# Optimization experiments

Measured on AMD Instinct MI355X. Metric: run time of the kernel, lower is better.

The kernel has to match this reference:

```python
import jax, jax.numpy as jnp
import numpy as np

NUM_EMBEDDINGS = 8192
EMBEDDING_DIM = 512
BATCH = 16384
COMMITMENT_COST = 0.25
EMBEDDING_SCALE = 0.1


def setup_inputs() -> dict:
    key = jax.random.key(0)
    k1, k2 = jax.random.split(key)
    x = jax.random.randint(k1, (BATCH,), 0, NUM_EMBEDDINGS, dtype=jnp.int64 if jax.config.jax_enable_x64 else jnp.int32)
    # codebook initialized uniform(-scale, scale) like the torch module
    W = jax.random.uniform(k2, (NUM_EMBEDDINGS, EMBEDDING_DIM), dtype=jnp.float32,
                           minval=-EMBEDDING_SCALE, maxval=EMBEDDING_SCALE)
    return {"x": x, "W": W}


def reference(x, W):
    # x: (B,) int indices into codebook; W: (K, D) codebook
    x_emb = W[x]                                           # (B, D) gather
    # squared euclidean distances via ||a||^2 + ||b||^2 - 2 a.b  -> (B, K)
    distances = ((x_emb ** 2).sum(axis=1, keepdims=True)
                 + (W ** 2).sum(axis=1)
                 - 2.0 * jnp.einsum('bd,kd->bk', x_emb, W))
    assignments = jnp.argmin(distances, axis=1)            # (B,)
    quantized = W[assignments]                             # (B, D)
    diff = quantized - x_emb                               # (B, D)
    loss = (diff ** 2).sum(axis=1).mean()
    loss = loss + COMMITMENT_COST * (W ** 2).sum()
    return (loss, quantized, diff)
```

## Files before the change

### kernel.cpp

```cpp
#include <hip/hip_runtime.h>

#define NUM_EMB    8192
#define EMB_DIM    512
#define BATCH_N    16384
#define BD         (BATCH_N * EMB_DIM)
#define TOTAL_OUT  (2 * BD + 1)
#define NCHUNK     (TOTAL_OUT / 4)
#define QCHUNK_END (BD / 4)
#define NBLOCKS    2048
#define NTHREADS   256
#define NTOTAL     (NBLOCKS * NTHREADS)

__device__ float g_partial[NBLOCKS];

__global__ __launch_bounds__(NTHREADS) void vq_sum(const float* __restrict__ W) {
    int tid = blockIdx.x * NTHREADS + threadIdx.x;
    const float4* W4 = (const float4*)W;
    float4 a = W4[tid];
    float4 b = W4[tid + NTOTAL];
    float s = a.x*a.x + a.y*a.y + a.z*a.z + a.w*a.w
            + b.x*b.x + b.y*b.y + b.z*b.z + b.w*b.w;
#pragma unroll
    for (int off = 32; off > 0; off >>= 1) s += __shfl_down(s, off, 64);
    __shared__ float ls[NTHREADS / 64];
    if ((threadIdx.x & 63) == 0) ls[threadIdx.x >> 6] = s;
    __syncthreads();
    if (threadIdx.x == 0) g_partial[blockIdx.x] = ls[0] + ls[1] + ls[2] + ls[3];
}

__global__ __launch_bounds__(NTHREADS) void vq_write(const int* __restrict__ x,
        const float* __restrict__ W, float* __restrict__ out) {
    const int tid  = blockIdx.x * NTHREADS + threadIdx.x;
    const int lane = threadIdx.x & 63;
    const int wave = (tid >> 6);
    float4* out4 = (float4*)out;

    const int b0 = 2 * wave;
    const int b1 = 2 * wave + 1;

    int k0 = x[b0];
    int k1 = x[b1];
    int kp = (b0 > 0) ? x[b0 - 1] : 0;

#pragma unroll
    for (int k = 0; k < 4; ++k) {
        int c = QCHUNK_END + 1 + tid + k * NTOTAL;
        if (c < NCHUNK) out4[c] = make_float4(0.f, 0.f, 0.f, 0.f);
    }
    if (blockIdx.x == 1 && threadIdx.x == 0) {
        out[TOTAL_OUT - 1] = 0.0f;
        float w = W[x[BATCH_N - 1] * EMB_DIM + 511];
        out4[QCHUNK_END] = make_float4(w, 0.f, 0.f, 0.f);
    }

    const float4* R0 = (const float4*)(W + k0 * EMB_DIM);
    const float4* R1 = (const float4*)(W + k1 * EMB_DIM);
    float4 a0 = R0[2 * lane], a1 = R0[2 * lane + 1];
    float4 c0 = R1[2 * lane], c1 = R1[2 * lane + 1];
    float p0 = W[kp * EMB_DIM + 511];
    float p1 = W[k0 * EMB_DIM + 511];

    {
        float pw = __shfl_up(a1.w, 1, 64);
        float first = (lane == 0) ? p0 : pw;
        int cb = 128 * b0;
        if (b0 != 0 || lane != 0)
            out4[cb + 2 * lane]     = make_float4(first, a0.x, a0.y, a0.z);
        out4[cb + 2 * lane + 1]     = make_float4(a0.w,  a1.x, a1.y, a1.z);
    }
    {
        float pw = __shfl_up(c1.w, 1, 64);
        float first = (lane == 0) ? p1 : pw;
        int cb = 128 * b1;
        out4[cb + 2 * lane]         = make_float4(first, c0.x, c0.y, c0.z);
        out4[cb + 2 * lane + 1]     = make_float4(c0.w,  c1.x, c1.y, c1.z);
    }

    if (blockIdx.x == 0) {
        __shared__ float red[NTHREADS];
        float s = 0.0f;
        for (int i = threadIdx.x; i < NBLOCKS; i += NTHREADS) s += g_partial[i];
        red[threadIdx.x] = s;
        __syncthreads();
        for (int st = NTHREADS / 2; st > 0; st >>= 1) {
            if (threadIdx.x < st) red[threadIdx.x] += red[threadIdx.x + st];
            __syncthreads();
        }
        if (threadIdx.x == 0) {
            float loss = 0.25f * red[0];
            int k = x[0];
            float4 v = *(const float4*)(W + k * EMB_DIM);
            out4[0] = make_float4(loss, v.x, v.y, v.z);
        }
    }
}

extern "C" void kernel_launch(void* const* d_in, const int* in_sizes, int n_in,
                              void* d_out, int out_size, void* d_ws, size_t ws_size,
                              hipStream_t stream) {
    const int*   x = (const int*)d_in[0];
    const float* W = (const float*)d_in[1];
    float* out     = (float*)d_out;

    vq_sum<<<NBLOCKS, NTHREADS, 0, stream>>>(W);
    vq_write<<<NBLOCKS, NTHREADS, 0, stream>>>(x, W, out);
}
```

Measured before the change: 94.85 us.

## Fuse codebook-norm reduction into write kernel via last-block atomic reduction

Merges the separate sum-of-squares kernel into the output-writing kernel. Each block stores its partial sum, then bumps an atomic counter, and the last block to finish does the final reduction and writes the loss. This removes a kernel launch and the dependency between the two kernels. It also switches the large output writes to nontemporal stores, and gets the previous row's last element with a wave shuffle instead of a global load. The costs are atomic traffic on one global counter and reliance on that counter being reset correctly between calls.

```diff
diff --git a/kernel.cpp b/kernel.cpp
--- a/kernel.cpp
+++ b/kernel.cpp
@@ -12,27 +12,21 @@
 #define NTOTAL     (NBLOCKS * NTHREADS)
 
 __device__ float g_partial[NBLOCKS];
+__device__ int   g_done;
 
-__global__ __launch_bounds__(NTHREADS) void vq_sum(const float* __restrict__ W) {
-    int tid = blockIdx.x * NTHREADS + threadIdx.x;
-    const float4* W4 = (const float4*)W;
-    float4 a = W4[tid];
-    float4 b = W4[tid + NTOTAL];
-    float s = a.x*a.x + a.y*a.y + a.z*a.z + a.w*a.w
-            + b.x*b.x + b.y*b.y + b.z*b.z + b.w*b.w;
-#pragma unroll
-    for (int off = 32; off > 0; off >>= 1) s += __shfl_down(s, off, 64);
-    __shared__ float ls[NTHREADS / 64];
-    if ((threadIdx.x & 63) == 0) ls[threadIdx.x >> 6] = s;
-    __syncthreads();
-    if (threadIdx.x == 0) g_partial[blockIdx.x] = ls[0] + ls[1] + ls[2] + ls[3];
+typedef float nf4 __attribute__((ext_vector_type(4)));
+__device__ __forceinline__ void nt_store4(float a, float b, float c, float d,
+                                          float4* p) {
+    nf4 v = {a, b, c, d};
+    __builtin_nontemporal_store(v, (nf4*)p);
 }
 
-__global__ __launch_bounds__(NTHREADS) void vq_write(const int* __restrict__ x,
+__global__ __launch_bounds__(NTHREADS) void vq_fused(const int* __restrict__ x,
         const float* __restrict__ W, float* __restrict__ out) {
     const int tid  = blockIdx.x * NTHREADS + threadIdx.x;
     const int lane = threadIdx.x & 63;
-    const int wave = (tid >> 6);
+    const int wid  = threadIdx.x >> 6;
+    const int wave = tid >> 6;
     float4* out4 = (float4*)out;
 
     const int b0 = 2 * wave;
@@ -42,10 +36,15 @@
     int k1 = x[b1];
     int kp = (b0 > 0) ? x[b0 - 1] : 0;
 
+    const float4* W4 = (const float4*)W;
+    float4 sa = W4[tid];
+    float4 sb = W4[tid + NTOTAL];
+
 #pragma unroll
     for (int k = 0; k < 4; ++k) {
         int c = QCHUNK_END + 1 + tid + k * NTOTAL;
-        if (c < NCHUNK) out4[c] = make_float4(0.f, 0.f, 0.f, 0.f);
+        if (c < NCHUNK)
+            nt_store4(0.f, 0.f, 0.f, 0.f, &out4[c]);
     }
     if (blockIdx.x == 1 && threadIdx.x == 0) {
         out[TOTAL_OUT - 1] = 0.0f;
@@ -58,29 +57,49 @@
     float4 a0 = R0[2 * lane], a1 = R0[2 * lane + 1];
     float4 c0 = R1[2 * lane], c1 = R1[2 * lane + 1];
     float p0 = W[kp * EMB_DIM + 511];
-    float p1 = W[k0 * EMB_DIM + 511];
+
+    float s = sa.x*sa.x + sa.y*sa.y + sa.z*sa.z + sa.w*sa.w
+            + sb.x*sb.x + sb.y*sb.y + sb.z*sb.z + sb.w*sb.w;
+#pragma unroll
+    for (int off = 32; off > 0; off >>= 1) s += __shfl_down(s, off, 64);
+    __shared__ float ls[NTHREADS / 64];
+    if (lane == 0) ls[wid] = s;
 
     {
         float pw = __shfl_up(a1.w, 1, 64);
         float first = (lane == 0) ? p0 : pw;
         int cb = 128 * b0;
         if (b0 != 0 || lane != 0)
-            out4[cb + 2 * lane]     = make_float4(first, a0.x, a0.y, a0.z);
-        out4[cb + 2 * lane + 1]     = make_float4(a0.w,  a1.x, a1.y, a1.z);
+            nt_store4(first, a0.x, a0.y, a0.z, &out4[cb + 2 * lane]);
+        nt_store4(a0.w, a1.x, a1.y, a1.z, &out4[cb + 2 * lane + 1]);
     }
     {
+        float p1 = __shfl(a1.w, 63, 64);
         float pw = __shfl_up(c1.w, 1, 64);
         float first = (lane == 0) ? p1 : pw;
         int cb = 128 * b1;
-        out4[cb + 2 * lane]         = make_float4(first, c0.x, c0.y, c0.z);
-        out4[cb + 2 * lane + 1]     = make_float4(c0.w,  c1.x, c1.y, c1.z);
+        nt_store4(first, c0.x, c0.y, c0.z, &out4[cb + 2 * lane]);
+        nt_store4(c0.w, c1.x, c1.y, c1.z, &out4[cb + 2 * lane + 1]);
     }
 
-    if (blockIdx.x == 0) {
+    __syncthreads();
+    __shared__ int lastflag;
+    if (threadIdx.x == 0) {
+        float part = ls[0] + ls[1] + ls[2] + ls[3];
+        __hip_atomic_store(&g_partial[blockIdx.x], part,
+                           __ATOMIC_RELEASE, __HIP_MEMORY_SCOPE_AGENT);
+        int t = __hip_atomic_fetch_add(&g_done, 1,
+                                       __ATOMIC_ACQ_REL, __HIP_MEMORY_SCOPE_AGENT);
+        lastflag = (t == NBLOCKS - 1);
+    }
+    __syncthreads();
+    if (lastflag) {
+        float s2 = 0.f;
+        for (int i = threadIdx.x; i < NBLOCKS; i += NTHREADS)
+            s2 += __hip_atomic_load(&g_partial[i], __ATOMIC_RELAXED,
+                                    __HIP_MEMORY_SCOPE_AGENT);
         __shared__ float red[NTHREADS];
-        float s = 0.0f;
-        for (int i = threadIdx.x; i < NBLOCKS; i += NTHREADS) s += g_partial[i];
-        red[threadIdx.x] = s;
+        red[threadIdx.x] = s2;
         __syncthreads();
         for (int st = NTHREADS / 2; st > 0; st >>= 1) {
             if (threadIdx.x < st) red[threadIdx.x] += red[threadIdx.x + st];
@@ -91,6 +110,8 @@
             int k = x[0];
             float4 v = *(const float4*)(W + k * EMB_DIM);
             out4[0] = make_float4(loss, v.x, v.y, v.z);
+            __hip_atomic_store(&g_done, 0,
+                               __ATOMIC_RELAXED, __HIP_MEMORY_SCOPE_AGENT);
         }
     }
 }
@@ -102,6 +123,5 @@
     const float* W = (const float*)d_in[1];
     float* out     = (float*)d_out;
 
-    vq_sum<<<NBLOCKS, NTHREADS, 0, stream>>>(W);
-    vq_write<<<NBLOCKS, NTHREADS, 0, stream>>>(x, W, out);
+    vq_fused<<<NBLOCKS, NTHREADS, 0, stream>>>(x, W, out);
 }
```

Result: slower. 299.8 us (+216.1%).
